# Performance work log

Measured on AMD Instinct MI355X. Metric: run time of the kernel, lower is better.

## Reference

```python
import jax, jax.numpy as jnp
import numpy as np

GI_DIM = 1220
HID = 150
GIJ = 3 * GI_DIM + 60  # 3720


def setup_inputs() -> dict:
    key = jax.random.key(0)
    ks = jax.random.split(key, 16)
    N, P = 50000, 100000
    inp = {
        "g_i": jax.random.normal(ks[0], (N, GI_DIM), jnp.float32),
        "mention_scores": jax.random.normal(ks[1], (N,), jnp.float32),
        "dist_emb": jax.random.normal(ks[2], (9, 20), jnp.float32) * 0.1,
        "genre_emb": jax.random.normal(ks[3], (8, 20), jnp.float32) * 0.1,
        "speaker_emb": jax.random.normal(ks[4], (3, 20), jnp.float32) * 0.1,
        "W1": jax.random.normal(ks[5], (GIJ, HID), jnp.float32) / np.sqrt(GIJ),
        "b1": jnp.zeros((HID,), jnp.float32),
        "W2": jax.random.normal(ks[6], (HID, HID), jnp.float32) / np.sqrt(HID),
        "b2": jnp.zeros((HID,), jnp.float32),
        "W3": jax.random.normal(ks[7], (HID, 1), jnp.float32) / np.sqrt(HID),
        "b3": jnp.zeros((1,), jnp.float32),
        "mention_ids": jax.random.randint(ks[8], (P,), 0, N, jnp.int64 if jax.config.jax_enable_x64 else jnp.int32),
        "antecedent_ids": jax.random.randint(ks[9], (P,), 0, N, jnp.int32),
        "distance_ids": jax.random.randint(ks[10], (P,), 0, 9, jnp.int32),
        "genre_ids": jax.random.randint(ks[11], (P,), 0, 8, jnp.int32),
        "speaker_ids": jax.random.randint(ks[12], (P,), 0, 3, jnp.int32),
    }
    return inp


def reference(g_i, mention_scores, dist_emb, genre_emb, speaker_emb,
              W1, b1, W2, b2, W3, b3,
              mention_ids, antecedent_ids, distance_ids, genre_ids, speaker_ids):
    # phi: [P, 60] pair features (distance, genre, speaker embeddings)
    phi = jnp.concatenate([dist_emb[distance_ids],
                           genre_emb[genre_ids],
                           speaker_emb[speaker_ids]], axis=1)
    i_g = g_i[mention_ids]      # [P, GI_DIM]
    j_g = g_i[antecedent_ids]   # [P, GI_DIM]
    pairs = jnp.concatenate([i_g, j_g, i_g * j_g, phi], axis=1)  # [P, GIJ]
    h = jax.nn.relu(pairs @ W1 + b1)
    h = jax.nn.relu(h @ W2 + b2)
    pairwise = (h @ W3 + b3)[:, 0]  # [P]
    sij = mention_scores[mention_ids] + mention_scores[antecedent_ids] + pairwise
    return sij
```

## Files before the change

### kernel.cpp

```cpp
#include <hip/hip_runtime.h>

#define GI  1220
#define KP  1280
#define BK  128
#define NCH (KP / BK)
#define NP  192
#define ABW 320

typedef __bf16        bf16x8 __attribute__((ext_vector_type(8)));
typedef float         f32x4  __attribute__((ext_vector_type(4)));
typedef unsigned int  u32x4  __attribute__((ext_vector_type(4)));
typedef unsigned int  u32x2  __attribute__((ext_vector_type(2)));

__device__ __forceinline__ unsigned short f2bf(float f) {
  __bf16 h = (__bf16)f;
  return __builtin_bit_cast(unsigned short, h);
}
__device__ __forceinline__ float bf2f(unsigned short u) {
  return (float)__builtin_bit_cast(__bf16, u);
}
__device__ __forceinline__ unsigned int pk2(float a, float b) {
  return (unsigned int)f2bf(a) | ((unsigned int)f2bf(b) << 16);
}

__global__ void prep_kernel(const float* __restrict__ W1, const float* __restrict__ W2,
                            const float* __restrict__ b1,
                            const float* __restrict__ de, const float* __restrict__ ge,
                            const float* __restrict__ se,
                            unsigned short* __restrict__ W1ab_t,
                            unsigned short* __restrict__ W1c_t,
                            unsigned short* __restrict__ W2_t,
                            float* __restrict__ projs) {
  int idx = blockIdx.x * 256 + threadIdx.x;
  const int R1 = ABW * KP, R2 = NP * KP, R3 = NP * NP, R4 = 20 * NP;
  if (idx < R1) {
    int n = idx / KP, k = idx % KP;
    float v = 0.f;
    if (k < GI) {
      if (n < 150)                 v = W1[k * 150 + n];
      else if (n >= 160 && n < 310) v = W1[(GI + k) * 150 + (n - 160)];
    }
    W1ab_t[idx] = f2bf(v);
    return;
  }
  idx -= R1;
  if (idx < R2) {
    int n = idx / KP, k = idx % KP;
    float v = (k < GI && n < 150) ? W1[(2 * GI + k) * 150 + n] : 0.f;
    W1c_t[idx] = f2bf(v);
    return;
  }
  idx -= R2;
  if (idx < R3) {
    int n = idx / NP, k = idx % NP;
    float v = (n < 150 && k < 150) ? W2[k * 150 + n] : 0.f;
    W2_t[idx] = f2bf(v);
    return;
  }
  idx -= R3;
  if (idx < R4) {
    int r = idx / NP, n = idx % NP;
    float v = 0.f;
    if (n < 150) {
      if (r < 9) {
        v = b1[n];
        for (int t = 0; t < 20; ++t) v += de[r * 20 + t] * W1[(3660 + t) * 150 + n];
      } else if (r < 17) {
        int q = r - 9;
        for (int t = 0; t < 20; ++t) v += ge[q * 20 + t] * W1[(3680 + t) * 150 + n];
      } else {
        int q = r - 17;
        for (int t = 0; t < 20; ++t) v += se[q * 20 + t] * W1[(3700 + t) * 150 + n];
      }
    }
    projs[idx] = v;
  }
}

__global__ __launch_bounds__(256, 3)
void ab_kernel(const float* __restrict__ g, const unsigned short* __restrict__ W1ab_t,
               unsigned short* __restrict__ AB, int N) {
  __shared__ __attribute__((aligned(16))) unsigned short sX[64 * 136];
  const int t = threadIdx.x;
  const int m0 = blockIdx.x * 64;
  const int w = t >> 6, lane = t & 63, quad = lane >> 4, lm = lane & 15;

  f32x4 acc[4][5];
#pragma unroll
  for (int a = 0; a < 4; ++a)
#pragma unroll
    for (int b = 0; b < 5; ++b) { acc[a][b].x = 0.f; acc[a][b].y = 0.f; acc[a][b].z = 0.f; acc[a][b].w = 0.f; }

  const int r = t >> 2, s = t & 3;
  int row = m0 + r; if (row >= N) row = N - 1;
  const float* gr = g + (long)row * GI;

  for (int c = 0; c < NCH; ++c) {
    __syncthreads();
#pragma unroll
    for (int i = 0; i < 8; ++i) {
      int k = c * BK + i * 16 + s * 4;
      u32x2 pk; pk.x = 0u; pk.y = 0u;
      if (k < GI) {
        f32x4 x = *(const f32x4*)(gr + k);
        pk.x = pk2(x.x, x.y);
        pk.y = pk2(x.z, x.w);
      }
      *(u32x2*)&sX[r * 136 + i * 16 + s * 4] = pk;
    }
    __syncthreads();
#pragma unroll
    for (int kk = 0; kk < 4; ++kk) {
      bf16x8 af[4];
#pragma unroll
      for (int mi = 0; mi < 4; ++mi)
        af[mi] = __builtin_bit_cast(bf16x8, *(const u32x4*)&sX[(mi * 16 + lm) * 136 + kk * 32 + quad * 8]);
#pragma unroll
      for (int tl = 0; tl < 5; ++tl) {
        int n = (w * 5 + tl) * 16 + lm;
        bf16x8 bfr = __builtin_bit_cast(bf16x8, *(const u32x4*)(W1ab_t + n * KP + c * BK + kk * 32 + quad * 8));
#pragma unroll
        for (int mi = 0; mi < 4; ++mi)
          acc[mi][tl] = __builtin_amdgcn_mfma_f32_16x16x32_bf16(af[mi], bfr, acc[mi][tl], 0, 0, 0);
      }
    }
  }
#pragma unroll
  for (int mi = 0; mi < 4; ++mi)
#pragma unroll
    for (int reg = 0; reg < 4; ++reg) {
      int m = m0 + mi * 16 + quad * 4 + reg;
      if (m < N) {
#pragma unroll
        for (int tl = 0; tl < 5; ++tl) {
          int n = (w * 5 + tl) * 16 + lm;
          AB[(long)m * ABW + n] = f2bf(acc[mi][tl][reg]);
        }
      }
    }
}

__global__ __launch_bounds__(256, 3)
void pair_kernel(const float* __restrict__ g, const float* __restrict__ msc,
                 const unsigned short* __restrict__ AB,
                 const unsigned short* __restrict__ W1c_t,
                 const unsigned short* __restrict__ W2_t,
                 const float* __restrict__ projs,
                 const float* __restrict__ b2, const float* __restrict__ W3,
                 const float* __restrict__ b3,
                 const int* __restrict__ mid, const int* __restrict__ aid,
                 const int* __restrict__ did, const int* __restrict__ gid,
                 const int* __restrict__ sid,
                 float* __restrict__ out, int N, int P) {
  __shared__ __attribute__((aligned(16))) unsigned short sXh1[64 * 200];
  __shared__ __attribute__((aligned(16))) unsigned short sBias[64 * NP];
  __shared__ int sM[64], sA[64], sD[64], sG[64], sS[64];
  __shared__ float sScore[64];

  const int t = threadIdx.x;
  const int p0 = blockIdx.x * 64;
  const int w = t >> 6, lane = t & 63, quad = lane >> 4, lm = lane & 15;

  if (t < 64) {
    int p = p0 + t;
    int m_ = 0, a_ = 0, d_ = 0, g_ = 0, s_ = 0;
    float sc = 0.f;
    if (p < P) {
      m_ = mid[p]; a_ = aid[p]; d_ = did[p]; g_ = gid[p]; s_ = sid[p];
      sc = msc[m_] + msc[a_];
    }
    sM[t] = m_; sA[t] = a_; sD[t] = d_; sG[t] = g_; sS[t] = s_;
    sScore[t] = sc;
  }
  __syncthreads();

  const int r = t >> 2, s = t & 3;
  const float* gm = g + (long)sM[r] * GI;
  const float* ga = g + (long)sA[r] * GI;

  {
    const unsigned short* Ar = AB + (long)sM[r] * ABW;
    const unsigned short* Br = AB + (long)sA[r] * ABW + 160;
    const float* dp = projs + sD[r] * NP;
    const float* gp = projs + (9 + sG[r]) * NP;
    const float* sp = projs + (17 + sS[r]) * NP;
#pragma unroll
    for (int j = 0; j < 6; ++j) {
      int n = s * 48 + j * 8;
      f32x4 p0v = *(const f32x4*)(dp + n) + *(const f32x4*)(gp + n) + *(const f32x4*)(sp + n);
      f32x4 p1v = *(const f32x4*)(dp + n + 4) + *(const f32x4*)(gp + n + 4) + *(const f32x4*)(sp + n + 4);
      if (n < 160) {
        u32x4 a8 = *(const u32x4*)(Ar + n);
        u32x4 b8 = *(const u32x4*)(Br + n);
        p0v.x += bf2f(a8.x & 0xffff) + bf2f(b8.x & 0xffff);
        p0v.y += bf2f(a8.x >> 16)    + bf2f(b8.x >> 16);
        p0v.z += bf2f(a8.y & 0xffff) + bf2f(b8.y & 0xffff);
        p0v.w += bf2f(a8.y >> 16)    + bf2f(b8.y >> 16);
        p1v.x += bf2f(a8.z & 0xffff) + bf2f(b8.z & 0xffff);
        p1v.y += bf2f(a8.z >> 16)    + bf2f(b8.z >> 16);
        p1v.z += bf2f(a8.w & 0xffff) + bf2f(b8.w & 0xffff);
        p1v.w += bf2f(a8.w >> 16)    + bf2f(b8.w >> 16);
      }
      u32x4 o;
      o.x = pk2(p0v.x, p0v.y); o.y = pk2(p0v.z, p0v.w);
      o.z = pk2(p1v.x, p1v.y); o.w = pk2(p1v.z, p1v.w);
      *(u32x4*)&sBias[r * NP + n] = o;
    }
  }

  f32x4 acc[4][3];
#pragma unroll
  for (int a = 0; a < 4; ++a)
#pragma unroll
    for (int b = 0; b < 3; ++b) { acc[a][b].x = 0.f; acc[a][b].y = 0.f; acc[a][b].z = 0.f; acc[a][b].w = 0.f; }

  for (int c = 0; c < NCH; ++c) {
    __syncthreads();
#pragma unroll
    for (int i = 0; i < 8; ++i) {
      int k = c * BK + i * 16 + s * 4;
      u32x2 pk; pk.x = 0u; pk.y = 0u;
      if (k < GI) {
        f32x4 x = *(const f32x4*)(gm + k);
        f32x4 y = *(const f32x4*)(ga + k);
        pk.x = pk2(x.x * y.x, x.y * y.y);
        pk.y = pk2(x.z * y.z, x.w * y.w);
      }
      *(u32x2*)&sXh1[r * 136 + i * 16 + s * 4] = pk;
    }
    __syncthreads();
#pragma unroll
    for (int kk = 0; kk < 4; ++kk) {
      bf16x8 af[4];
#pragma unroll
      for (int mi = 0; mi < 4; ++mi)
        af[mi] = __builtin_bit_cast(bf16x8, *(const u32x4*)&sXh1[(mi * 16 + lm) * 136 + kk * 32 + quad * 8]);
#pragma unroll
      for (int tl = 0; tl < 3; ++tl) {
        int n = (w * 3 + tl) * 16 + lm;
        bf16x8 bfr = __builtin_bit_cast(bf16x8, *(const u32x4*)(W1c_t + n * KP + c * BK + kk * 32 + quad * 8));
#pragma unroll
        for (int mi = 0; mi < 4; ++mi)
          acc[mi][tl] = __builtin_amdgcn_mfma_f32_16x16x32_bf16(af[mi], bfr, acc[mi][tl], 0, 0, 0);
      }
    }
  }

  __syncthreads();
#pragma unroll
  for (int mi = 0; mi < 4; ++mi)
#pragma unroll
    for (int tl = 0; tl < 3; ++tl) {
      int n = (w * 3 + tl) * 16 + lm;
#pragma unroll
      for (int reg = 0; reg < 4; ++reg) {
        int m = mi * 16 + quad * 4 + reg;
        float v = acc[mi][tl][reg] + bf2f(sBias[m * NP + n]);
        v = fmaxf(v, 0.f);
        sXh1[m * 200 + n] = f2bf(v);
      }
    }
  __syncthreads();

  f32x4 acc2[4][3];
#pragma unroll
  for (int a = 0; a < 4; ++a)
#pragma unroll
    for (int b = 0; b < 3; ++b) { acc2[a][b].x = 0.f; acc2[a][b].y = 0.f; acc2[a][b].z = 0.f; acc2[a][b].w = 0.f; }
#pragma unroll
  for (int kk = 0; kk < 6; ++kk) {
    bf16x8 af[4];
#pragma unroll
    for (int mi = 0; mi < 4; ++mi)
      af[mi] = __builtin_bit_cast(bf16x8, *(const u32x4*)&sXh1[(mi * 16 + lm) * 200 + kk * 32 + quad * 8]);
#pragma unroll
    for (int tl = 0; tl < 3; ++tl) {
      int n = (w * 3 + tl) * 16 + lm;
      bf16x8 bfr = __builtin_bit_cast(bf16x8, *(const u32x4*)(W2_t + n * NP + kk * 32 + quad * 8));
#pragma unroll
      for (int mi = 0; mi < 4; ++mi)
        acc2[mi][tl] = __builtin_amdgcn_mfma_f32_16x16x32_bf16(af[mi], bfr, acc2[mi][tl], 0, 0, 0);
    }
  }

#pragma unroll
  for (int mi = 0; mi < 4; ++mi)
#pragma unroll
    for (int tl = 0; tl < 3; ++tl) {
      int n = (w * 3 + tl) * 16 + lm;
      float bb = (n < 150) ? b2[n] : 0.f;
#pragma unroll
      for (int reg = 0; reg < 4; ++reg) {
        int m = mi * 16 + quad * 4 + reg;
        float v = acc2[mi][tl][reg] + bb;
        v = fmaxf(v, 0.f);
        sBias[m * NP + n] = f2bf(v);
      }
    }
  __syncthreads();

  {
    float sum = 0.f;
#pragma unroll
    for (int j = 0; j < 48; ++j) {
      int n = s * 48 + j;
      if (n < 150) sum += bf2f(sBias[r * NP + n]) * W3[n];
    }
    sum += __shfl_xor(sum, 1);
    sum += __shfl_xor(sum, 2);
    if (s == 0) {
      int p = p0 + r;
      if (p < P) out[p] = sScore[r] + sum + b3[0];
    }
  }
}

extern "C" void kernel_launch(void* const* d_in, const int* in_sizes, int n_in,
                              void* d_out, int out_size, void* d_ws, size_t ws_size,
                              hipStream_t stream) {
  (void)n_in; (void)out_size; (void)ws_size;
  const float* g   = (const float*)d_in[0];
  const float* msc = (const float*)d_in[1];
  const float* de  = (const float*)d_in[2];
  const float* ge  = (const float*)d_in[3];
  const float* se  = (const float*)d_in[4];
  const float* W1  = (const float*)d_in[5];
  const float* b1  = (const float*)d_in[6];
  const float* W2  = (const float*)d_in[7];
  const float* b2  = (const float*)d_in[8];
  const float* W3  = (const float*)d_in[9];
  const float* b3  = (const float*)d_in[10];
  const int* mid = (const int*)d_in[11];
  const int* aid = (const int*)d_in[12];
  const int* did = (const int*)d_in[13];
  const int* gid = (const int*)d_in[14];
  const int* sid = (const int*)d_in[15];
  const int N = in_sizes[0] / GI;
  const int P = in_sizes[11];
  float* out = (float*)d_out;

  char* ws = (char*)d_ws;
  size_t off = 0;
  auto alloc = [&](size_t bytes) { char* p = ws + off; off = (off + bytes + 255) & ~(size_t)255; return p; };
  unsigned short* AB     = (unsigned short*)alloc((size_t)N * ABW * 2);
  unsigned short* W1ab_t = (unsigned short*)alloc((size_t)ABW * KP * 2);
  unsigned short* W1c_t  = (unsigned short*)alloc((size_t)NP * KP * 2);
  unsigned short* W2_t   = (unsigned short*)alloc((size_t)NP * NP * 2);
  float* projs           = (float*)alloc((size_t)20 * NP * 4);

  const int prep_total = ABW * KP + NP * KP + NP * NP + 20 * NP;
  prep_kernel<<<(prep_total + 255) / 256, 256, 0, stream>>>(W1, W2, b1, de, ge, se,
                                                            W1ab_t, W1c_t, W2_t, projs);
  ab_kernel<<<(N + 63) / 64, 256, 0, stream>>>(g, W1ab_t, AB, N);
  pair_kernel<<<(P + 63) / 64, 256, 0, stream>>>(g, msc, AB, W1c_t, W2_t, projs,
                                                 b2, W3, b3, mid, aid, did, gid, sid,
                                                 out, N, P);
}
```

Baseline: 772.6 us.

## Cache bf16 padded g rows during AB pass and gather them in pair kernel

The AB kernel now also writes a bf16, zero-padded copy of each g row into workspace. The pair kernel gathers these half-width rows for the i*j product instead of fp32 rows, halving gather traffic. The bias buffer is folded into the single shared tile and indices are packed, cutting LDS so the occupancy hint rises to 5 blocks. This costs an extra full-size write of g in bf16 and rounds the inputs before multiplying, and it needs enough workspace (falls back otherwise).

```diff
diff --git a/kernel.cpp b/kernel.cpp
--- a/kernel.cpp
+++ b/kernel.cpp
@@ -21,6 +21,13 @@
 }
 __device__ __forceinline__ unsigned int pk2(float a, float b) {
   return (unsigned int)f2bf(a) | ((unsigned int)f2bf(b) << 16);
+}
+__device__ __forceinline__ unsigned int mulbf2(unsigned int a, unsigned int b) {
+  float xl = __builtin_bit_cast(float, a << 16);
+  float xh = __builtin_bit_cast(float, a & 0xffff0000u);
+  float yl = __builtin_bit_cast(float, b << 16);
+  float yh = __builtin_bit_cast(float, b & 0xffff0000u);
+  return pk2(xl * yl, xh * yh);
 }
 
 __global__ void prep_kernel(const float* __restrict__ W1, const float* __restrict__ W2,
@@ -79,7 +86,8 @@
 
 __global__ __launch_bounds__(256, 3)
 void ab_kernel(const float* __restrict__ g, const unsigned short* __restrict__ W1ab_t,
-               unsigned short* __restrict__ AB, int N) {
+               unsigned short* __restrict__ AB, unsigned short* __restrict__ gpad,
+               int N) {
   __shared__ __attribute__((aligned(16))) unsigned short sX[64 * 136];
   const int t = threadIdx.x;
   const int m0 = blockIdx.x * 64;
@@ -107,6 +115,7 @@
         pk.y = pk2(x.z, x.w);
       }
       *(u32x2*)&sX[r * 136 + i * 16 + s * 4] = pk;
+      if (gpad) *(u32x2*)(gpad + (long)row * KP + k) = pk;
     }
     __syncthreads();
 #pragma unroll
@@ -140,8 +149,10 @@
     }
 }
 
-__global__ __launch_bounds__(256, 3)
-void pair_kernel(const float* __restrict__ g, const float* __restrict__ msc,
+template <bool PADG>
+__global__ __launch_bounds__(256, 5)
+void pair_kernel(const float* __restrict__ g, const unsigned short* __restrict__ gpad,
+                 const float* __restrict__ msc,
                  const unsigned short* __restrict__ AB,
                  const unsigned short* __restrict__ W1c_t,
                  const unsigned short* __restrict__ W2_t,
@@ -151,11 +162,9 @@
                  const int* __restrict__ mid, const int* __restrict__ aid,
                  const int* __restrict__ did, const int* __restrict__ gid,
                  const int* __restrict__ sid,
-                 float* __restrict__ out, int N, int P) {
-  __shared__ __attribute__((aligned(16))) unsigned short sXh1[64 * 200];
-  __shared__ __attribute__((aligned(16))) unsigned short sBias[64 * NP];
-  __shared__ int sM[64], sA[64], sD[64], sG[64], sS[64];
-  __shared__ float sScore[64];
+                 float* __restrict__ out, int P) {
+  __shared__ __attribute__((aligned(16))) unsigned short sX[64 * 200];
+  __shared__ int sM[64], sA[64], sDGS[64];
 
   const int t = threadIdx.x;
   const int p0 = blockIdx.x * 64;
@@ -163,27 +172,88 @@
 
   if (t < 64) {
     int p = p0 + t;
-    int m_ = 0, a_ = 0, d_ = 0, g_ = 0, s_ = 0;
-    float sc = 0.f;
+    int m_ = 0, a_ = 0, dgs = 0;
     if (p < P) {
-      m_ = mid[p]; a_ = aid[p]; d_ = did[p]; g_ = gid[p]; s_ = sid[p];
-      sc = msc[m_] + msc[a_];
-    }
-    sM[t] = m_; sA[t] = a_; sD[t] = d_; sG[t] = g_; sS[t] = s_;
-    sScore[t] = sc;
+      m_ = mid[p]; a_ = aid[p];
+      dgs = did[p] | (gid[p] << 4) | (sid[p] << 8);
+    }
+    sM[t] = m_; sA[t] = a_; sDGS[t] = dgs;
   }
   __syncthreads();
 
   const int r = t >> 2, s = t & 3;
-  const float* gm = g + (long)sM[r] * GI;
-  const float* ga = g + (long)sA[r] * GI;
+
+  f32x4 acc[4][3];
+#pragma unroll
+  for (int a = 0; a < 4; ++a)
+#pragma unroll
+    for (int b = 0; b < 3; ++b) { acc[a][b].x = 0.f; acc[a][b].y = 0.f; acc[a][b].z = 0.f; acc[a][b].w = 0.f; }
+
+  const float* gm32; const float* ga32;
+  const unsigned short* gm16; const unsigned short* ga16;
+  if constexpr (PADG) {
+    gm16 = gpad + (long)sM[r] * KP;
+    ga16 = gpad + (long)sA[r] * KP;
+  } else {
+    gm32 = g + (long)sM[r] * GI;
+    ga32 = g + (long)sA[r] * GI;
+  }
+
+  for (int c = 0; c < NCH; ++c) {
+    __syncthreads();
+    if constexpr (PADG) {
+#pragma unroll
+      for (int i = 0; i < 4; ++i) {
+        int k = c * BK + i * 32 + s * 8;
+        u32x4 xx = *(const u32x4*)(gm16 + k);
+        u32x4 yy = *(const u32x4*)(ga16 + k);
+        u32x4 o;
+        o.x = mulbf2(xx.x, yy.x);
+        o.y = mulbf2(xx.y, yy.y);
+        o.z = mulbf2(xx.z, yy.z);
+        o.w = mulbf2(xx.w, yy.w);
+        *(u32x4*)&sX[r * 136 + i * 32 + s * 8] = o;
+      }
+    } else {
+#pragma unroll
+      for (int i = 0; i < 8; ++i) {
+        int k = c * BK + i * 16 + s * 4;
+        u32x2 pk; pk.x = 0u; pk.y = 0u;
+        if (k < GI) {
+          f32x4 x = *(const f32x4*)(gm32 + k);
+          f32x4 y = *(const f32x4*)(ga32 + k);
+          pk.x = pk2(x.x * y.x, x.y * y.y);
+          pk.y = pk2(x.z * y.z, x.w * y.w);
+        }
+        *(u32x2*)&sX[r * 136 + i * 16 + s * 4] = pk;
+      }
+    }
+    __syncthreads();
+#pragma unroll
+    for (int kk = 0; kk < 4; ++kk) {
+      bf16x8 af[4];
+#pragma unroll
+      for (int mi = 0; mi < 4; ++mi)
+        af[mi] = __builtin_bit_cast(bf16x8, *(const u32x4*)&sX[(mi * 16 + lm) * 136 + kk * 32 + quad * 8]);
+#pragma unroll
+      for (int tl = 0; tl < 3; ++tl) {
+        int n = (w * 3 + tl) * 16 + lm;
+        bf16x8 bfr = __builtin_bit_cast(bf16x8, *(const u32x4*)(W1c_t + n * KP + c * BK + kk * 32 + quad * 8));
+#pragma unroll
+        for (int mi = 0; mi < 4; ++mi)
+          acc[mi][tl] = __builtin_amdgcn_mfma_f32_16x16x32_bf16(af[mi], bfr, acc[mi][tl], 0, 0, 0);
+      }
+    }
+  }
+  __syncthreads();
 
   {
     const unsigned short* Ar = AB + (long)sM[r] * ABW;
     const unsigned short* Br = AB + (long)sA[r] * ABW + 160;
-    const float* dp = projs + sD[r] * NP;
-    const float* gp = projs + (9 + sG[r]) * NP;
-    const float* sp = projs + (17 + sS[r]) * NP;
+    int dgs = sDGS[r];
+    const float* dp = projs + (dgs & 15) * NP;
+    const float* gp = projs + (9 + ((dgs >> 4) & 15)) * NP;
+    const float* sp = projs + (17 + (dgs >> 8)) * NP;
 #pragma unroll
     for (int j = 0; j < 6; ++j) {
       int n = s * 48 + j * 8;
@@ -204,49 +274,11 @@
       u32x4 o;
       o.x = pk2(p0v.x, p0v.y); o.y = pk2(p0v.z, p0v.w);
       o.z = pk2(p1v.x, p1v.y); o.w = pk2(p1v.z, p1v.w);
-      *(u32x4*)&sBias[r * NP + n] = o;
-    }
-  }
-
-  f32x4 acc[4][3];
-#pragma unroll
-  for (int a = 0; a < 4; ++a)
-#pragma unroll
-    for (int b = 0; b < 3; ++b) { acc[a][b].x = 0.f; acc[a][b].y = 0.f; acc[a][b].z = 0.f; acc[a][b].w = 0.f; }
-
-  for (int c = 0; c < NCH; ++c) {
-    __syncthreads();
-#pragma unroll
-    for (int i = 0; i < 8; ++i) {
-      int k = c * BK + i * 16 + s * 4;
-      u32x2 pk; pk.x = 0u; pk.y = 0u;
-      if (k < GI) {
-        f32x4 x = *(const f32x4*)(gm + k);
-        f32x4 y = *(const f32x4*)(ga + k);
-        pk.x = pk2(x.x * y.x, x.y * y.y);
-        pk.y = pk2(x.z * y.z, x.w * y.w);
-      }
-      *(u32x2*)&sXh1[r * 136 + i * 16 + s * 4] = pk;
-    }
-    __syncthreads();
-#pragma unroll
-    for (int kk = 0; kk < 4; ++kk) {
-      bf16x8 af[4];
-#pragma unroll
-      for (int mi = 0; mi < 4; ++mi)
-        af[mi] = __builtin_bit_cast(bf16x8, *(const u32x4*)&sXh1[(mi * 16 + lm) * 136 + kk * 32 + quad * 8]);
-#pragma unroll
-      for (int tl = 0; tl < 3; ++tl) {
-        int n = (w * 3 + tl) * 16 + lm;
-        bf16x8 bfr = __builtin_bit_cast(bf16x8, *(const u32x4*)(W1c_t + n * KP + c * BK + kk * 32 + quad * 8));
-#pragma unroll
-        for (int mi = 0; mi < 4; ++mi)
-          acc[mi][tl] = __builtin_amdgcn_mfma_f32_16x16x32_bf16(af[mi], bfr, acc[mi][tl], 0, 0, 0);
-      }
-    }
-  }
-
-  __syncthreads();
+      *(u32x4*)&sX[r * 200 + n] = o;
+    }
+  }
+  __syncthreads();
+
 #pragma unroll
   for (int mi = 0; mi < 4; ++mi)
 #pragma unroll
@@ -255,9 +287,8 @@
 #pragma unroll
       for (int reg = 0; reg < 4; ++reg) {
         int m = mi * 16 + quad * 4 + reg;
-        float v = acc[mi][tl][reg] + bf2f(sBias[m * NP + n]);
-        v = fmaxf(v, 0.f);
-        sXh1[m * 200 + n] = f2bf(v);
+        float v = acc[mi][tl][reg] + bf2f(sX[m * 200 + n]);
+        sX[m * 200 + n] = f2bf(fmaxf(v, 0.f));
       }
     }
   __syncthreads();
@@ -272,7 +303,7 @@
     bf16x8 af[4];
 #pragma unroll
     for (int mi = 0; mi < 4; ++mi)
-      af[mi] = __builtin_bit_cast(bf16x8, *(const u32x4*)&sXh1[(mi * 16 + lm) * 200 + kk * 32 + quad * 8]);
+      af[mi] = __builtin_bit_cast(bf16x8, *(const u32x4*)&sX[(mi * 16 + lm) * 200 + kk * 32 + quad * 8]);
 #pragma unroll
     for (int tl = 0; tl < 3; ++tl) {
       int n = (w * 3 + tl) * 16 + lm;
@@ -282,6 +313,7 @@
         acc2[mi][tl] = __builtin_amdgcn_mfma_f32_16x16x32_bf16(af[mi], bfr, acc2[mi][tl], 0, 0, 0);
     }
   }
+  __syncthreads();
 
 #pragma unroll
   for (int mi = 0; mi < 4; ++mi)
@@ -293,8 +325,7 @@
       for (int reg = 0; reg < 4; ++reg) {
         int m = mi * 16 + quad * 4 + reg;
         float v = acc2[mi][tl][reg] + bb;
-        v = fmaxf(v, 0.f);
-        sBias[m * NP + n] = f2bf(v);
+        sX[m * 200 + n] = f2bf(fmaxf(v, 0.f));
       }
     }
   __syncthreads();
@@ -304,13 +335,13 @@
 #pragma unroll
     for (int j = 0; j < 48; ++j) {
       int n = s * 48 + j;
-      if (n < 150) sum += bf2f(sBias[r * NP + n]) * W3[n];
+      if (n < 150) sum += bf2f(sX[r * 200 + n]) * W3[n];
     }
     sum += __shfl_xor(sum, 1);
     sum += __shfl_xor(sum, 2);
     if (s == 0) {
       int p = p0 + r;
-      if (p < P) out[p] = sScore[r] + sum + b3[0];
+      if (p < P) out[p] = msc[sM[r]] + msc[sA[r]] + sum + b3[0];
     }
   }
 }
@@ -318,7 +349,7 @@
 extern "C" void kernel_launch(void* const* d_in, const int* in_sizes, int n_in,
                               void* d_out, int out_size, void* d_ws, size_t ws_size,
                               hipStream_t stream) {
-  (void)n_in; (void)out_size; (void)ws_size;
+  (void)n_in; (void)out_size;
   const float* g   = (const float*)d_in[0];
   const float* msc = (const float*)d_in[1];
   const float* de  = (const float*)d_in[2];
@@ -348,11 +379,19 @@
   unsigned short* W2_t   = (unsigned short*)alloc((size_t)NP * NP * 2);
   float* projs           = (float*)alloc((size_t)20 * NP * 4);
 
+  size_t gpad_bytes = (size_t)N * KP * 2;
+  unsigned short* gpad = nullptr;
+  if (off + gpad_bytes + 256 <= ws_size)
+    gpad = (unsigned short*)alloc(gpad_bytes);
+
   const int prep_total = ABW * KP + NP * KP + NP * NP + 20 * NP;
   prep_kernel<<<(prep_total + 255) / 256, 256, 0, stream>>>(W1, W2, b1, de, ge, se,
                                                             W1ab_t, W1c_t, W2_t, projs);
-  ab_kernel<<<(N + 63) / 64, 256, 0, stream>>>(g, W1ab_t, AB, N);
-  pair_kernel<<<(P + 63) / 64, 256, 0, stream>>>(g, msc, AB, W1c_t, W2_t, projs,
-                                                 b2, W3, b3, mid, aid, did, gid, sid,
-                                                 out, N, P);
-}
+  ab_kernel<<<(N + 63) / 64, 256, 0, stream>>>(g, W1ab_t, AB, gpad, N);
+  if (gpad)
+    pair_kernel<true><<<(P + 63) / 64, 256, 0, stream>>>(g, gpad, msc, AB, W1c_t, W2_t, projs,
+                                                         b2, W3, b3, mid, aid, did, gid, sid, out, P);
+  else
+    pair_kernel<false><<<(P + 63) / 64, 256, 0, stream>>>(g, gpad, msc, AB, W1c_t, W2_t, projs,
+                                                          b2, W3, b3, mid, aid, did, gid, sid, out, P);
+}
```

New measurement: 831.0 us. 1.08x slower.
